# Kernel optimization log

Measured on AMD Instinct MI355X. Metric: run time of the kernel, lower is better.

The kernel has to match this reference:

```python
import jax, jax.numpy as jnp
import numpy as np

NUM_GRAPHS = 1024
N_NODES = 8388608

def setup_inputs() -> dict:
    key = jax.random.key(0)
    k1, k2, k3 = jax.random.split(key, 3)
    positions = jax.random.normal(k1, (N_NODES, 3), dtype=jnp.float32)
    q = jax.random.normal(k2, (N_NODES,), dtype=jnp.float32)
    batch = jnp.sort(jax.random.randint(k3, (N_NODES,), 0, NUM_GRAPHS, dtype=jnp.int64))
    return {"positions": positions, "q": q, "batch": batch}

def reference(positions, q, batch):
    # q: [N] -> [N,1]; remove global mean over all nodes (remove_mean=True)
    qc = q[:, None] - jnp.mean(q)
    # per-graph polarization: sum_i q_i * r_i  -> [NUM_GRAPHS, 3]
    pol = jax.ops.segment_sum(qc * positions, batch, num_segments=NUM_GRAPHS)
    return pol
```

## Files before the change

### kernel.cpp

```cpp
#include <hip/hip_runtime.h>


#define N_NODES         8388608
#define NUM_GRAPHS      1024
#define BLK             256
#define NODES_PER_BLOCK 4096
#define NBLOCKS         (N_NODES / NODES_PER_BLOCK)
#define ITER            4
#define NSLOT           4

#define IBASE_OFF       16
#define REC_OFF         2064
#define REC_STRIDE      32
#define EXTRA_OFF       (REC_OFF + NBLOCKS * REC_STRIDE)
#define WS_FLOATS       (EXTRA_OFF + NUM_GRAPHS * 6)

__device__ __forceinline__ void flush_seg(int id, int base,
                                          float qx, float qy, float qz,
                                          float rx, float ry, float rz,
                                          float* sslot, float* extra) {
    int s = id - base;
    if (s < NSLOT) {
        atomicAdd(&sslot[s * 6 + 0], qx); atomicAdd(&sslot[s * 6 + 1], qy);
        atomicAdd(&sslot[s * 6 + 2], qz); atomicAdd(&sslot[s * 6 + 3], rx);
        atomicAdd(&sslot[s * 6 + 4], ry); atomicAdd(&sslot[s * 6 + 5], rz);
    } else {
        atomicAdd(&extra[id * 6 + 0], qx); atomicAdd(&extra[id * 6 + 1], qy);
        atomicAdd(&extra[id * 6 + 2], qz); atomicAdd(&extra[id * 6 + 3], rx);
        atomicAdd(&extra[id * 6 + 4], ry); atomicAdd(&extra[id * 6 + 5], rz);
    }
}

__global__ __launch_bounds__(BLK) void pol_main(const float4* __restrict__ p4,
                                                const float4* __restrict__ q4,
                                                const int4*   __restrict__ b4,
                                                const int*    __restrict__ batch,
                                                float* __restrict__ ws) {
    __shared__ float sslot[NSLOT * 6];
    __shared__ float sqsum;

    const int t = threadIdx.x;
    const int b = blockIdx.x;
    float* extra = ws + EXTRA_OFF;

    if (t == 0) sqsum = 0.f;
    if (t < NSLOT * 6) sslot[t] = 0.f;
    const int base = batch[b * NODES_PER_BLOCK];
    __syncthreads();

    int idA = -1, idB = -1;
    float aqx = 0, aqy = 0, aqz = 0, arx = 0, ary = 0, arz = 0;
    float bqx = 0, bqy = 0, bqz = 0, brx = 0, bry = 0, brz = 0;
    float qsum = 0.f;

    const int blk_v4 = b * (NODES_PER_BLOCK / 4);

    #pragma unroll
    for (int j = 0; j < ITER; ++j) {
        int vi = blk_v4 + j * BLK + t;
        float4 qv = q4[vi];
        int4   bv = b4[vi];
        float4 p0 = p4[3 * vi + 0];
        float4 p1 = p4[3 * vi + 1];
        float4 p2 = p4[3 * vi + 2];

        float qs[4] = {qv.x, qv.y, qv.z, qv.w};
        int   ids[4] = {bv.x, bv.y, bv.z, bv.w};
        float px[4] = {p0.x, p0.w, p1.z, p2.y};
        float py[4] = {p0.y, p1.x, p1.w, p2.z};
        float pz[4] = {p0.z, p1.y, p2.x, p2.w};

        #pragma unroll
        for (int k = 0; k < 4; ++k) {
            float qj = qs[k];
            int   id = ids[k];
            qsum += qj;
            if (id == idA) {
                aqx = fmaf(qj, px[k], aqx); aqy = fmaf(qj, py[k], aqy); aqz = fmaf(qj, pz[k], aqz);
                arx += px[k]; ary += py[k]; arz += pz[k];
            } else if (id == idB) {
                bqx = fmaf(qj, px[k], bqx); bqy = fmaf(qj, py[k], bqy); bqz = fmaf(qj, pz[k], bqz);
                brx += px[k]; bry += py[k]; brz += pz[k];
            } else if (idA < 0) {
                idA = id;
                aqx = qj * px[k]; aqy = qj * py[k]; aqz = qj * pz[k];
                arx = px[k]; ary = py[k]; arz = pz[k];
            } else if (idB < 0) {
                idB = id;
                bqx = qj * px[k]; bqy = qj * py[k]; bqz = qj * pz[k];
                brx = px[k]; bry = py[k]; brz = pz[k];
            } else {
                atomicAdd(&extra[idA * 6 + 0], aqx); atomicAdd(&extra[idA * 6 + 1], aqy);
                atomicAdd(&extra[idA * 6 + 2], aqz); atomicAdd(&extra[idA * 6 + 3], arx);
                atomicAdd(&extra[idA * 6 + 4], ary); atomicAdd(&extra[idA * 6 + 5], arz);
                idA = id;
                aqx = qj * px[k]; aqy = qj * py[k]; aqz = qj * pz[k];
                arx = px[k]; ary = py[k]; arz = pz[k];
            }
        }
    }

    #pragma unroll
    for (int off = 32; off > 0; off >>= 1) qsum += __shfl_down(qsum, off, 64);
    if ((t & 63) == 0) atomicAdd(&sqsum, qsum);

    bool uniA = __all(idA == __shfl(idA, 0, 64));
    if (uniA) {
        #pragma unroll
        for (int off = 32; off > 0; off >>= 1) {
            aqx += __shfl_down(aqx, off, 64); aqy += __shfl_down(aqy, off, 64);
            aqz += __shfl_down(aqz, off, 64); arx += __shfl_down(arx, off, 64);
            ary += __shfl_down(ary, off, 64); arz += __shfl_down(arz, off, 64);
        }
        if ((t & 63) == 0) flush_seg(idA, base, aqx, aqy, aqz, arx, ary, arz, sslot, extra);
    } else {
        flush_seg(idA, base, aqx, aqy, aqz, arx, ary, arz, sslot, extra);
    }

    unsigned long long mB = __ballot(idB >= 0);
    if (mB) {
        bool allB  = (mB == ~0ull);
        int  firstB = __shfl(idB, 0, 64);
        bool uniB  = allB && __all(idB == firstB);
        if (uniB) {
            #pragma unroll
            for (int off = 32; off > 0; off >>= 1) {
                bqx += __shfl_down(bqx, off, 64); bqy += __shfl_down(bqy, off, 64);
                bqz += __shfl_down(bqz, off, 64); brx += __shfl_down(brx, off, 64);
                bry += __shfl_down(bry, off, 64); brz += __shfl_down(brz, off, 64);
            }
            if ((t & 63) == 0) flush_seg(idB, base, bqx, bqy, bqz, brx, bry, brz, sslot, extra);
        } else if (idB >= 0) {
            flush_seg(idB, base, bqx, bqy, bqz, brx, bry, brz, sslot, extra);
        }
    }
    __syncthreads();

    float* rec = ws + REC_OFF + (size_t)b * REC_STRIDE;
    if (t == 0) {
        rec[0] = sqsum;
        ((int*)(ws + IBASE_OFF))[b] = base;
    }
    if (t < NSLOT * 6) rec[8 + t] = sslot[t];
}

__global__ __launch_bounds__(1024) void finalize_kernel(const float* __restrict__ ws,
                                                        float* __restrict__ out) {
    __shared__ float sm[16];
    __shared__ float smean;
    const int t = threadIdx.x;

    float s = ws[REC_OFF + (size_t)t * REC_STRIDE]
            + ws[REC_OFF + (size_t)(t + 1024) * REC_STRIDE];
    #pragma unroll
    for (int off = 32; off > 0; off >>= 1) s += __shfl_down(s, off, 64);
    if ((t & 63) == 0) sm[t >> 6] = s;
    __syncthreads();
    if (t == 0) {
        float tot = 0.f;
        #pragma unroll
        for (int i = 0; i < 16; ++i) tot += sm[i];
        smean = tot * (1.0f / (float)N_NODES);
    }
    __syncthreads();
    const float mean = smean;

    const int g = t;
    const int* ibase = (const int*)(ws + IBASE_OFF);
    const float* extra = ws + EXTRA_OFF;

    float qx = extra[g * 6 + 0], qy = extra[g * 6 + 1], qz = extra[g * 6 + 2];
    float rx = extra[g * 6 + 3], ry = extra[g * 6 + 4], rz = extra[g * 6 + 5];

    int lo = 0, hi = NBLOCKS - 1, B = -1;
    while (lo <= hi) {
        int mid = (lo + hi) >> 1;
        if (ibase[mid] <= g) { B = mid; lo = mid + 1; } else hi = mid - 1;
    }
    for (int b = B; b >= 0; --b) {
        int sl = g - ibase[b];
        if (sl >= NSLOT) break;
        const float* p = ws + REC_OFF + (size_t)b * REC_STRIDE + 8 + sl * 6;
        qx += p[0]; qy += p[1]; qz += p[2];
        rx += p[3]; ry += p[4]; rz += p[5];
    }
    out[g * 3 + 0] = fmaf(-mean, rx, qx);
    out[g * 3 + 1] = fmaf(-mean, ry, qy);
    out[g * 3 + 2] = fmaf(-mean, rz, qz);
}


__global__ void sum_q_kernel(const float* __restrict__ q, float* __restrict__ ws, int n4) {
    int tid = blockIdx.x * blockDim.x + threadIdx.x;
    int stride = gridDim.x * blockDim.x;
    const float4* q4 = (const float4*)q;
    float s = 0.f;
    for (int i = tid; i < n4; i += stride) {
        float4 v = q4[i];
        s += (v.x + v.y) + (v.z + v.w);
    }
    for (int off = 32; off > 0; off >>= 1) s += __shfl_down(s, off, 64);
    __shared__ float smem[4];
    int lane = threadIdx.x & 63, wave = threadIdx.x >> 6;
    if (lane == 0) smem[wave] = s;
    __syncthreads();
    if (threadIdx.x == 0) atomicAdd(ws, (smem[0] + smem[1]) + (smem[2] + smem[3]));
}

__global__ void pol_atomic_kernel(const float* __restrict__ pos,
                                  const float* __restrict__ q,
                                  const int*   __restrict__ batch,
                                  const float* __restrict__ ws,
                                  float* __restrict__ out, int n) {
    const float mean = ws[0] * (1.0f / (float)N_NODES);
    int tid = blockIdx.x * blockDim.x + threadIdx.x;
    int stride = gridDim.x * blockDim.x;
    int n4 = n >> 2;
    const float4* q4 = (const float4*)q;
    const int4*   b4 = (const int4*)batch;
    const float4* p4 = (const float4*)pos;

    for (int i = tid; i < n4; i += stride) {
        float4 qv = q4[i];
        int4   bv = b4[i];
        float4 p0 = p4[3 * i + 0];
        float4 p1 = p4[3 * i + 1];
        float4 p2 = p4[3 * i + 2];
        float qs[4] = {qv.x - mean, qv.y - mean, qv.z - mean, qv.w - mean};
        int  ids[4] = {bv.x, bv.y, bv.z, bv.w};
        float px[4] = {p0.x, p0.w, p1.z, p2.y};
        float py[4] = {p0.y, p1.x, p1.w, p2.z};
        float pz[4] = {p0.z, p1.y, p2.x, p2.w};
        int cur = ids[0];
        float sx = 0.f, sy = 0.f, sz = 0.f;
        #pragma unroll
        for (int j = 0; j < 4; ++j) {
            if (ids[j] != cur) {
                atomicAdd(&out[cur * 3 + 0], sx);
                atomicAdd(&out[cur * 3 + 1], sy);
                atomicAdd(&out[cur * 3 + 2], sz);
                sx = sy = sz = 0.f;
                cur = ids[j];
            }
            sx = fmaf(qs[j], px[j], sx);
            sy = fmaf(qs[j], py[j], sy);
            sz = fmaf(qs[j], pz[j], sz);
        }
        int first = __shfl(cur, 0, 64);
        bool uniform = __all(cur == first);
        if (uniform) {
            for (int off = 32; off > 0; off >>= 1) {
                sx += __shfl_down(sx, off, 64);
                sy += __shfl_down(sy, off, 64);
                sz += __shfl_down(sz, off, 64);
            }
            if ((threadIdx.x & 63) == 0) {
                atomicAdd(&out[cur * 3 + 0], sx);
                atomicAdd(&out[cur * 3 + 1], sy);
                atomicAdd(&out[cur * 3 + 2], sz);
            }
        } else {
            atomicAdd(&out[cur * 3 + 0], sx);
            atomicAdd(&out[cur * 3 + 1], sy);
            atomicAdd(&out[cur * 3 + 2], sz);
        }
    }
}

extern "C" void kernel_launch(void* const* d_in, const int* in_sizes, int n_in,
                              void* d_out, int out_size, void* d_ws, size_t ws_size,
                              hipStream_t stream) {
    const float* pos   = (const float*)d_in[0];
    const float* q     = (const float*)d_in[1];
    const int*   batch = (const int*)d_in[2];
    float* out = (float*)d_out;
    float* ws  = (float*)d_ws;
    int n = in_sizes[1];

    if (ws_size >= (size_t)WS_FLOATS * sizeof(float)) {
        hipMemsetAsync(ws + EXTRA_OFF, 0, (size_t)NUM_GRAPHS * 6 * sizeof(float), stream);
        pol_main<<<NBLOCKS, BLK, 0, stream>>>((const float4*)pos, (const float4*)q,
                                              (const int4*)batch, batch, ws);
        finalize_kernel<<<1, 1024, 0, stream>>>(ws, out);
    } else {
        hipMemsetAsync(d_out, 0, (size_t)out_size * sizeof(float), stream);
        hipMemsetAsync(d_ws, 0, sizeof(float), stream);
        sum_q_kernel<<<4096, BLK, 0, stream>>>(q, ws, n >> 2);
        pol_atomic_kernel<<<8192, BLK, 0, stream>>>(pos, q, batch, ws, out, n);
    }
}
```

Measured before the change: 210.3 us.

## Replace per-node batch reads with per-block binary search for the segment split

```diff
diff --git a/kernel.cpp b/kernel.cpp
--- a/kernel.cpp
+++ b/kernel.cpp
@@ -15,87 +15,96 @@
 #define EXTRA_OFF       (REC_OFF + NBLOCKS * REC_STRIDE)
 #define WS_FLOATS       (EXTRA_OFF + NUM_GRAPHS * 6)
 
-__device__ __forceinline__ void flush_seg(int id, int base,
-                                          float qx, float qy, float qz,
-                                          float rx, float ry, float rz,
-                                          float* sslot, float* extra) {
-    int s = id - base;
-    if (s < NSLOT) {
-        atomicAdd(&sslot[s * 6 + 0], qx); atomicAdd(&sslot[s * 6 + 1], qy);
-        atomicAdd(&sslot[s * 6 + 2], qz); atomicAdd(&sslot[s * 6 + 3], rx);
-        atomicAdd(&sslot[s * 6 + 4], ry); atomicAdd(&sslot[s * 6 + 5], rz);
-    } else {
-        atomicAdd(&extra[id * 6 + 0], qx); atomicAdd(&extra[id * 6 + 1], qy);
-        atomicAdd(&extra[id * 6 + 2], qz); atomicAdd(&extra[id * 6 + 3], rx);
-        atomicAdd(&extra[id * 6 + 4], ry); atomicAdd(&extra[id * 6 + 5], rz);
-    }
-}
-
 __global__ __launch_bounds__(BLK) void pol_main(const float4* __restrict__ p4,
                                                 const float4* __restrict__ q4,
-                                                const int4*   __restrict__ b4,
                                                 const int*    __restrict__ batch,
                                                 float* __restrict__ ws) {
     __shared__ float sslot[NSLOT * 6];
     __shared__ float sqsum;
+    __shared__ int   sh_i0, sh_i1, sh_split;
 
     const int t = threadIdx.x;
     const int b = blockIdx.x;
     float* extra = ws + EXTRA_OFF;
 
-    if (t == 0) sqsum = 0.f;
+    const int s = b * NODES_PER_BLOCK;
+    const int e = s + NODES_PER_BLOCK;
+
     if (t < NSLOT * 6) sslot[t] = 0.f;
-    const int base = batch[b * NODES_PER_BLOCK];
-    __syncthreads();
-
-    int idA = -1, idB = -1;
+    if (t == 0) {
+        sqsum = 0.f;
+        int i0 = batch[s];
+        int i1 = batch[e - 1];
+        int split = e;
+        if (i1 != i0) {
+            int lo = s + 1, hi = e - 1;
+            while (lo < hi) {
+                int mid = (lo + hi) >> 1;
+                if (batch[mid] > i0) hi = mid; else lo = mid + 1;
+            }
+            split = lo;
+        }
+        sh_i0 = i0; sh_i1 = i1; sh_split = split;
+    }
+    __syncthreads();
+    const int i0 = sh_i0, i1 = sh_i1, split = sh_split;
+    const bool general = (i1 > i0 + 1);
+
+    float4 Q[ITER], P0[ITER], P1[ITER], P2[ITER];
+    const int blk_v4 = b * (NODES_PER_BLOCK / 4);
+    #pragma unroll
+    for (int j = 0; j < ITER; ++j) {
+        int vi = blk_v4 + j * BLK + t;
+        Q[j]  = q4[vi];
+        P0[j] = p4[3 * vi + 0];
+        P1[j] = p4[3 * vi + 1];
+        P2[j] = p4[3 * vi + 2];
+    }
+
     float aqx = 0, aqy = 0, aqz = 0, arx = 0, ary = 0, arz = 0;
     float bqx = 0, bqy = 0, bqz = 0, brx = 0, bry = 0, brz = 0;
     float qsum = 0.f;
 
-    const int blk_v4 = b * (NODES_PER_BLOCK / 4);
-
-    #pragma unroll
-    for (int j = 0; j < ITER; ++j) {
-        int vi = blk_v4 + j * BLK + t;
-        float4 qv = q4[vi];
-        int4   bv = b4[vi];
-        float4 p0 = p4[3 * vi + 0];
-        float4 p1 = p4[3 * vi + 1];
-        float4 p2 = p4[3 * vi + 2];
-
-        float qs[4] = {qv.x, qv.y, qv.z, qv.w};
-        int   ids[4] = {bv.x, bv.y, bv.z, bv.w};
-        float px[4] = {p0.x, p0.w, p1.z, p2.y};
-        float py[4] = {p0.y, p1.x, p1.w, p2.z};
-        float pz[4] = {p0.z, p1.y, p2.x, p2.w};
-
-        #pragma unroll
-        for (int k = 0; k < 4; ++k) {
-            float qj = qs[k];
-            int   id = ids[k];
-            qsum += qj;
-            if (id == idA) {
-                aqx = fmaf(qj, px[k], aqx); aqy = fmaf(qj, py[k], aqy); aqz = fmaf(qj, pz[k], aqz);
-                arx += px[k]; ary += py[k]; arz += pz[k];
-            } else if (id == idB) {
-                bqx = fmaf(qj, px[k], bqx); bqy = fmaf(qj, py[k], bqy); bqz = fmaf(qj, pz[k], bqz);
-                brx += px[k]; bry += py[k]; brz += pz[k];
-            } else if (idA < 0) {
-                idA = id;
-                aqx = qj * px[k]; aqy = qj * py[k]; aqz = qj * pz[k];
-                arx = px[k]; ary = py[k]; arz = pz[k];
-            } else if (idB < 0) {
-                idB = id;
-                bqx = qj * px[k]; bqy = qj * py[k]; bqz = qj * pz[k];
-                brx = px[k]; bry = py[k]; brz = pz[k];
-            } else {
-                atomicAdd(&extra[idA * 6 + 0], aqx); atomicAdd(&extra[idA * 6 + 1], aqy);
-                atomicAdd(&extra[idA * 6 + 2], aqz); atomicAdd(&extra[idA * 6 + 3], arx);
-                atomicAdd(&extra[idA * 6 + 4], ary); atomicAdd(&extra[idA * 6 + 5], arz);
-                idA = id;
-                aqx = qj * px[k]; aqy = qj * py[k]; aqz = qj * pz[k];
-                arx = px[k]; ary = py[k]; arz = pz[k];
+    if (!general) {
+        #pragma unroll
+        for (int j = 0; j < ITER; ++j) {
+            int gidx = (blk_v4 + j * BLK + t) * 4;
+            float qs[4] = {Q[j].x, Q[j].y, Q[j].z, Q[j].w};
+            float px[4] = {P0[j].x, P0[j].w, P1[j].z, P2[j].y};
+            float py[4] = {P0[j].y, P1[j].x, P1[j].w, P2[j].z};
+            float pz[4] = {P0[j].z, P1[j].y, P2[j].x, P2[j].w};
+            qsum += (qs[0] + qs[1]) + (qs[2] + qs[3]);
+            #pragma unroll
+            for (int k = 0; k < 4; ++k) {
+                if (gidx + k < split) {
+                    aqx = fmaf(qs[k], px[k], aqx); aqy = fmaf(qs[k], py[k], aqy);
+                    aqz = fmaf(qs[k], pz[k], aqz);
+                    arx += px[k]; ary += py[k]; arz += pz[k];
+                } else {
+                    bqx = fmaf(qs[k], px[k], bqx); bqy = fmaf(qs[k], py[k], bqy);
+                    bqz = fmaf(qs[k], pz[k], bqz);
+                    brx += px[k]; bry += py[k]; brz += pz[k];
+                }
+            }
+        }
+    } else {
+        #pragma unroll
+        for (int j = 0; j < ITER; ++j) {
+            int gidx = (blk_v4 + j * BLK + t) * 4;
+            float qs[4] = {Q[j].x, Q[j].y, Q[j].z, Q[j].w};
+            float px[4] = {P0[j].x, P0[j].w, P1[j].z, P2[j].y};
+            float py[4] = {P0[j].y, P1[j].x, P1[j].w, P2[j].z};
+            float pz[4] = {P0[j].z, P1[j].y, P2[j].x, P2[j].w};
+            for (int k = 0; k < 4; ++k) {
+                int id = batch[gidx + k];
+                float qv = qs[k];
+                qsum += qv;
+                atomicAdd(&extra[id * 6 + 0], qv * px[k]);
+                atomicAdd(&extra[id * 6 + 1], qv * py[k]);
+                atomicAdd(&extra[id * 6 + 2], qv * pz[k]);
+                atomicAdd(&extra[id * 6 + 3], px[k]);
+                atomicAdd(&extra[id * 6 + 4], py[k]);
+                atomicAdd(&extra[id * 6 + 5], pz[k]);
             }
         }
     }
@@ -104,34 +113,31 @@
     for (int off = 32; off > 0; off >>= 1) qsum += __shfl_down(qsum, off, 64);
     if ((t & 63) == 0) atomicAdd(&sqsum, qsum);
 
-    bool uniA = __all(idA == __shfl(idA, 0, 64));
-    if (uniA) {
+    if (!general) {
         #pragma unroll
         for (int off = 32; off > 0; off >>= 1) {
             aqx += __shfl_down(aqx, off, 64); aqy += __shfl_down(aqy, off, 64);
             aqz += __shfl_down(aqz, off, 64); arx += __shfl_down(arx, off, 64);
             ary += __shfl_down(ary, off, 64); arz += __shfl_down(arz, off, 64);
         }
-        if ((t & 63) == 0) flush_seg(idA, base, aqx, aqy, aqz, arx, ary, arz, sslot, extra);
-    } else {
-        flush_seg(idA, base, aqx, aqy, aqz, arx, ary, arz, sslot, extra);
-    }
-
-    unsigned long long mB = __ballot(idB >= 0);
-    if (mB) {
-        bool allB  = (mB == ~0ull);
-        int  firstB = __shfl(idB, 0, 64);
-        bool uniB  = allB && __all(idB == firstB);
-        if (uniB) {
+        if ((t & 63) == 0) {
+            atomicAdd(&sslot[0], aqx); atomicAdd(&sslot[1], aqy);
+            atomicAdd(&sslot[2], aqz); atomicAdd(&sslot[3], arx);
+            atomicAdd(&sslot[4], ary); atomicAdd(&sslot[5], arz);
+        }
+        if (split < e) {
             #pragma unroll
             for (int off = 32; off > 0; off >>= 1) {
                 bqx += __shfl_down(bqx, off, 64); bqy += __shfl_down(bqy, off, 64);
                 bqz += __shfl_down(bqz, off, 64); brx += __shfl_down(brx, off, 64);
                 bry += __shfl_down(bry, off, 64); brz += __shfl_down(brz, off, 64);
             }
-            if ((t & 63) == 0) flush_seg(idB, base, bqx, bqy, bqz, brx, bry, brz, sslot, extra);
-        } else if (idB >= 0) {
-            flush_seg(idB, base, bqx, bqy, bqz, brx, bry, brz, sslot, extra);
+            if ((t & 63) == 0) {
+                int sl = i1 - i0;
+                atomicAdd(&sslot[sl * 6 + 0], bqx); atomicAdd(&sslot[sl * 6 + 1], bqy);
+                atomicAdd(&sslot[sl * 6 + 2], bqz); atomicAdd(&sslot[sl * 6 + 3], brx);
+                atomicAdd(&sslot[sl * 6 + 4], bry); atomicAdd(&sslot[sl * 6 + 5], brz);
+            }
         }
     }
     __syncthreads();
@@ -139,7 +145,7 @@
     float* rec = ws + REC_OFF + (size_t)b * REC_STRIDE;
     if (t == 0) {
         rec[0] = sqsum;
-        ((int*)(ws + IBASE_OFF))[b] = base;
+        ((int*)(ws + IBASE_OFF))[b] = i0;
     }
     if (t < NSLOT * 6) rec[8 + t] = sslot[t];
 }
@@ -280,7 +286,7 @@
     if (ws_size >= (size_t)WS_FLOATS * sizeof(float)) {
         hipMemsetAsync(ws + EXTRA_OFF, 0, (size_t)NUM_GRAPHS * 6 * sizeof(float), stream);
         pol_main<<<NBLOCKS, BLK, 0, stream>>>((const float4*)pos, (const float4*)q,
-                                              (const int4*)batch, batch, ws);
+                                              batch, ws);
         finalize_kernel<<<1, 1024, 0, stream>>>(ws, out);
     } else {
         hipMemsetAsync(d_out, 0, (size_t)out_size * sizeof(float), stream);
```

New measurement: 204.6 us. -2.7%, faster.
